# Kernel tuning notes

Measured on AMD Instinct MI355X. Metric: run time of the kernel, lower is better.

The kernel has to match this reference:

```python
import math
import jax, jax.numpy as jnp
import numpy as np

B, N, D, H, DR = 2, 1024, 1024, 16, 128  # batch, seq, dim, heads, router_dim
INIT_SCALE = 0.01   # CayleyLinear init_scale
TEMP = 1.0          # gate temperature (constant, not learnable)
TAU_D_INIT = math.log(math.expm1(0.1))  # softplus^-1(|tau_destructive|)


def setup_inputs() -> dict:
    key = jax.random.key(0)
    ks = jax.random.split(key, 6)
    x_re = jax.random.normal(ks[0], (B, N, D), jnp.float32)
    x_im = jax.random.normal(ks[1], (B, N, D), jnp.float32)
    Wq_re = jax.random.normal(ks[2], (H * DR, D), jnp.float32) * INIT_SCALE
    Wq_im = jax.random.normal(ks[3], (H * DR, D), jnp.float32) * INIT_SCALE
    Wk_re = jax.random.normal(ks[4], (H * DR, D), jnp.float32) * INIT_SCALE
    Wk_im = jax.random.normal(ks[5], (H * DR, D), jnp.float32) * INIT_SCALE
    w_destructive = jnp.full((1,), TAU_D_INIT, jnp.float32)
    return {"x_re": x_re, "x_im": x_im, "Wq_re": Wq_re, "Wq_im": Wq_im,
            "Wk_re": Wk_re, "Wk_im": Wk_im, "w_destructive": w_destructive}


def _qnormalize(z):
    # normalize_quantum_state: unit L2 norm of the complex state along last dim
    nrm = jnp.sqrt(jnp.sum(jnp.real(z) ** 2 + jnp.imag(z) ** 2, axis=-1, keepdims=True) + 1e-12)
    return z / nrm.astype(z.dtype)


def reference(x_re, x_im, Wq_re, Wq_im, Wk_re, Wk_im, w_destructive):
    x = jax.lax.complex(x_re, x_im)                 # (B, N, D) complex64
    Wq = jax.lax.complex(Wq_re, Wq_im)              # (H*DR, D)
    Wk = jax.lax.complex(Wk_re, Wk_im)
    # CayleyLinear projections, split heads: (B, N, H*DR) -> (B, H, N, DR)
    rQ = (x @ Wq.T).reshape(B, N, H, DR).transpose(0, 2, 1, 3)
    rK = (x @ Wk.T).reshape(B, N, H, DR).transpose(0, 2, 1, 3)
    rQ = _qnormalize(rQ)
    rK = _qnormalize(rK)
    # pairwise interference: 2 * Re(<q_i, k_j>) / d   -> (B, H, N, N) real
    inner = jnp.einsum('bhnd,bhmd->bhnm', jnp.conj(rQ), rK)
    inter = 2.0 * jnp.real(inner) / DR
    # SparseInterferenceGate, soft path (training=True): tau_d = -softplus(w_d)
    tau_d = -jax.nn.softplus(w_destructive[0])
    routing_weights = jax.nn.sigmoid((inter - tau_d) / (TEMP + 1e-06))
    return routing_weights
```

## Files before the change

### kernel.cpp

```cpp
#include <hip/hip_runtime.h>
#include <hip/hip_bf16.h>
#include <cstdint>


typedef int   i32x4  __attribute__((ext_vector_type(4)));
typedef float f32x4  __attribute__((ext_vector_type(4)));

#define MFMAI8(a, b, c) __builtin_amdgcn_mfma_i32_16x16x64_i8(a, b, c, 0, 0, 0)
#define BAR()   asm volatile("s_barrier" ::: "memory")
#define LGKM0() asm volatile("s_waitcnt lgkmcnt(0)" ::: "memory")
#define VM6()   asm volatile("s_waitcnt vmcnt(6)" ::: "memory")
#define VM4()   asm volatile("s_waitcnt vmcnt(4)" ::: "memory")
#define VM0()   asm volatile("s_waitcnt vmcnt(0)" ::: "memory")

#define XBOUND 5.8f
#define WBOUND 0.058f
#define XSB    8.2f
#define WSB    0.082f
#define QBOUND 3.2f

static __device__ __forceinline__ int q8(float x) {
  int i = (int)rintf(x);
  return i < -127 ? -127 : (i > 127 ? 127 : i);
}

static __device__ __forceinline__ void gload16(const void* g, void* l) {
  __builtin_amdgcn_global_load_lds(
      (const __attribute__((address_space(1))) void*)g,
      (__attribute__((address_space(3))) void*)l, 16, 0, 0);
}

static __device__ __forceinline__ unsigned pack4(int a, int b, int c, int d) {
  return (unsigned)(a & 255) | ((unsigned)(b & 255) << 8) |
         ((unsigned)(c & 255) << 16) | ((unsigned)(d & 255) << 24);
}

struct PackK {
  const float* srcA[3];
  const float* srcB[3];
  char* dA[3];
  char* dB[3];
  char* dS[3];
  float sa[3];
  float ss[3];
  float* ztab;
  int zn4;
};

__global__ __launch_bounds__(256) void pack_k_kernel(PackK jobs) {
  const int j = blockIdx.y;
  const int idx = blockIdx.x * 256 + threadIdx.x;
  if (j == 0 && idx < jobs.zn4) {
    *reinterpret_cast<float4*>(jobs.ztab + 4 * idx) = float4{0.f, 0.f, 0.f, 0.f};
  }
  const long o = (long)(idx >> 8) * 1024 + ((idx & 255) << 2);
  const float4 va = *reinterpret_cast<const float4*>(jobs.srcA[j] + o);
  const float4 vb = *reinterpret_cast<const float4*>(jobs.srcB[j] + o);
  const float sa = jobs.sa[j], ss = jobs.ss[j];
  *reinterpret_cast<unsigned*>(jobs.dA[j] + o) =
      pack4(q8(va.x * sa), q8(va.y * sa), q8(va.z * sa), q8(va.w * sa));
  *reinterpret_cast<unsigned*>(jobs.dB[j] + o) =
      pack4(q8(vb.x * sa), q8(vb.y * sa), q8(vb.z * sa), q8(vb.w * sa));
  *reinterpret_cast<unsigned*>(jobs.dS[j] + o) =
      pack4(q8((va.x + vb.x) * ss), q8((va.y + vb.y) * ss),
            q8((va.z + vb.z) * ss), q8((va.w + vb.w) * ss));
}

#define GEO_COMMON                                                             \
  const int tid  = threadIdx.x;                                                \
  const int wid  = tid >> 6;                                                   \
  const int lane = tid & 63;                                                   \
  const int wr = wid >> 2;                                                     \
  const int wc = wid & 3;                                                      \
  const int fr = lane & 15;                                                    \
  const int srow = wid * 8 + (lane >> 3);                                      \
  const int scol = ((lane & 7) ^ (lane >> 3)) << 4;                            \
  const int sxr = (lane & 7) << 4;                                             \
  const int cb0 = (((lane >> 4) << 4)) ^ sxr;                                  \
  const int cb1 = ((((lane >> 4) << 4)) + 64) ^ sxr;


#define KST(U, TILE, APAN, BPAN) do {                                          \
    const int _tl = (TILE);                                                    \
    if (_tl < 8) {                                                             \
      const char* _g = ((U) == 0 ? (APAN) : (BPAN) + ((U) - 1) * 131072)       \
                       + (long)srow * 1024 + _tl * 128 + scol;                 \
      char* _d = smem + (_tl & 1) * 49152 + (U) * 16384 + (wid << 10);         \
      gload16(_g, _d);                                                         \
      gload16(_g + 65536, _d + 8192);                                          \
    }                                                                          \
  } while (0)

#define MQ3(ACC, AV, R) do {                                                   \
    __builtin_amdgcn_s_setprio(1);                                             \
    _Pragma("unroll")                                                          \
    for (int _n = 0; _n < 4; _n++) {                                           \
      ACC[R][_n]       = MFMAI8(AV[0], b0[_n], ACC[R][_n]);                    \
      ACC[R][_n]       = MFMAI8(AV[1], b1[_n], ACC[R][_n]);                    \
      ACC[(R) + 1][_n] = MFMAI8(AV[2], b0[_n], ACC[(R) + 1][_n]);              \
      ACC[(R) + 1][_n] = MFMAI8(AV[3], b1[_n], ACC[(R) + 1][_n]);              \
    }                                                                          \
    __builtin_amdgcn_s_setprio(0);                                             \
  } while (0)

#define K3LOOP(ACC, APAN, BPAN)                                                \
  KST(0, 0, APAN, BPAN); KST(1, 0, APAN, BPAN); KST(2, 0, APAN, BPAN);         \
  KST(1, 1, APAN, BPAN); KST(2, 1, APAN, BPAN);                                \
  VM4(); BAR();                                                                \
  for (int t = 0; t < 8; ++t) {                                                \
    const char* cbuf = smem + (t & 1) * 49152;                                 \
    const char* pA = cbuf + (wr * 64 + fr) * 128;                              \
    const char* pB = cbuf + 16384 + (wc * 64 + fr) * 128;                      \
    i32x4 b0[4], b1[4], a0[4], a1[4];                                          \
    _Pragma("unroll")                                                          \
    for (int n = 0; n < 4; n++) {                                              \
      b0[n] = *(const i32x4*)(pB + n * 2048 + cb0);                            \
      b1[n] = *(const i32x4*)(pB + n * 2048 + cb1);                            \
    }                                                                          \
    a0[0] = *(const i32x4*)(pA + cb0);                                         \
    a0[1] = *(const i32x4*)(pA + cb1);                                         \
    a0[2] = *(const i32x4*)(pA + 2048 + cb0);                                  \
    a0[3] = *(const i32x4*)(pA + 2048 + cb1);                                  \
    KST(0, t + 1, APAN, BPAN);                                                 \
    BAR(); LGKM0();                                                            \
    MQ3(ACC, a0, 0);                                                           \
    BAR();                                                                     \
    a1[0] = *(const i32x4*)(pA + 4096 + cb0);                                  \
    a1[1] = *(const i32x4*)(pA + 4096 + cb1);                                  \
    a1[2] = *(const i32x4*)(pA + 6144 + cb0);                                  \
    a1[3] = *(const i32x4*)(pA + 6144 + cb1);                                  \
    KST(1, t + 2, APAN, BPAN); KST(2, t + 2, APAN, BPAN);                      \
    if (t <= 5)      { VM4(); }                                                \
    else if (t == 6) { VM0(); }                                                \
    BAR(); LGKM0();                                                            \
    MQ3(ACC, a1, 2);                                                           \
    BAR();                                                                     \
  }

#define EPI_PART(PART, EXPR) do {                                              \
    char* QKp = QpB + z * 8388608L + (PART) * 128;                             \
    float* STp = ssq + z * 32768;                                              \
    _Pragma("unroll")                                                          \
    for (int n = 0; n < 4; n++) {                                              \
      const int bn = n0 + wc * 64 + n * 16 + fr;                               \
      const int b = bn >> 10, nn = bn & 1023;                                  \
      const long rowbase = (((long)(b * 16 + hh)) * 1024 + nn) * 256;          \
      int ipr = 0;                                                             \
      _Pragma("unroll")                                                        \
      for (int mt = 0; mt < 4; mt++) {                                         \
        const int d0 = wr * 64 + mt * 16 + g * 4;                              \
        int iv0 = EXPR(mt, n, 0), iv1 = EXPR(mt, n, 1);                        \
        int iv2 = EXPR(mt, n, 2), iv3 = EXPR(mt, n, 3);                        \
        ipr += iv0 * iv0 + iv1 * iv1 + iv2 * iv2 + iv3 * iv3;                  \
        *reinterpret_cast<unsigned*>(QKp + rowbase + d0) =                     \
            pack4(iv0, iv1, iv2, iv3);                                         \
      }                                                                        \
      float s = (float)ipr;                                                    \
      s += __shfl_xor(s, 16);                                                  \
      s += __shfl_xor(s, 32);                                                  \
      if (g == 0) atomicAdd(&STp[(b * 16 + hh) * 1024 + nn], s);               \
    }                                                                          \
  } while (0)

#define EX_RE(mt, n, r) q8((float)accA[mt][n][r] * c1)
#define EX_IM(mt, n, r) q8((dq3f * (float)accA[mt][n][r] - fs[mt][n][r]) * oqv)

__global__ __launch_bounds__(512, 2)
void gemm_k3(const char* __restrict__ Wp, const char* __restrict__ Xp,
             char* __restrict__ QpB, float* __restrict__ ssq,
             float dqnf, float dq3f, float oqv, float c1) {
  __shared__ __attribute__((aligned(16))) char smem[98304];
  GEO_COMMON
  const int g = lane >> 4;
  const long z = blockIdx.z;
  const int m0 = blockIdx.y * 128;
  const int n0 = blockIdx.x * 256;
  const int hh = m0 >> 7;
  const long PL2 = 2097152;
  const char* Ar = Wp + (z * 3 + 0) * PL2 + (long)m0 * 1024;
  const char* Ai = Wp + (z * 3 + 1) * PL2 + (long)m0 * 1024;
  const char* As = Wp + (z * 3 + 2) * PL2 + (long)m0 * 1024;
  const char* Br = Xp + 0 * PL2 + (long)n0 * 1024;
  const char* Bi = Xp + 1 * PL2 + (long)n0 * 1024;
  const char* Bs = Xp + 2 * PL2 + (long)n0 * 1024;

  i32x4 accA[4][4] = {};
  K3LOOP(accA, Ar, Br)
  i32x4 accB[4][4] = {};
  K3LOOP(accB, Ai, Bi)

  f32x4 fs[4][4];
#pragma unroll
  for (int mt = 0; mt < 4; mt++)
#pragma unroll
    for (int n = 0; n < 4; n++) {
      f32x4 t;
#pragma unroll
      for (int r = 0; r < 4; r++)
        t[r] = dqnf * (float)(accA[mt][n][r] + accB[mt][n][r]);
      fs[mt][n] = t;
      accA[mt][n] -= accB[mt][n];
    }

  EPI_PART(0, EX_RE);

#pragma unroll
  for (int mt = 0; mt < 4; mt++)
#pragma unroll
    for (int n = 0; n < 4; n++) accA[mt][n] = i32x4{0, 0, 0, 0};

  K3LOOP(accA, As, Bs)

  EPI_PART(1, EX_IM);
}

#define STAGE(SEG, TILE) do {                                                  \
    const int _tl = (TILE);                                                    \
    if (_tl < NT) {                                                            \
      const char* _g = ((SEG) >= 2 ? Ag : Bg) +                                \
          (long)(((SEG) & 1) * 128 + srow) * ROWB + _tl * 128;                 \
      char* _d = smem + ((_tl & 1) << 16) + (((SEG) >= 2) ? 0 : 32768) +       \
                 (((SEG) & 1) << 14) + (wid << 10);                            \
      gload16(_g + scol, _d);                                                  \
      gload16(_g + (long)ROWB * 64 + scol, _d + 8192);                         \
    }                                                                          \
  } while (0)

#define RDQ(dst, Q) do {                                                       \
    const char* _p = pA + (Q) * 4096;                                          \
    dst[0] = *reinterpret_cast<const i32x4*>(_p + cb0);                        \
    dst[1] = *reinterpret_cast<const i32x4*>(_p + cb1);                        \
    dst[2] = *reinterpret_cast<const i32x4*>(_p + 2048 + cb0);                 \
    dst[3] = *reinterpret_cast<const i32x4*>(_p + 2048 + cb1);                 \
  } while (0)

#define MFMAQ(AV, R) do {                                                      \
    __builtin_amdgcn_s_setprio(1);                                             \
    _Pragma("unroll")                                                          \
    for (int _n = 0; _n < 4; _n++) {                                           \
      acc[R][_n]       = MFMAI8(AV[0], b0[_n], acc[R][_n]);                    \
      acc[R][_n]       = MFMAI8(AV[1], b1[_n], acc[R][_n]);                    \
      acc[(R) + 1][_n] = MFMAI8(AV[2], b0[_n], acc[(R) + 1][_n]);              \
      acc[(R) + 1][_n] = MFMAI8(AV[3], b1[_n], acc[(R) + 1][_n]);              \
    }                                                                          \
    __builtin_amdgcn_s_setprio(0);                                             \
  } while (0)

#define KLOOP()                                                                \
  STAGE(0, 0); STAGE(1, 0); STAGE(2, 0); STAGE(3, 0);                          \
  STAGE(0, 1); STAGE(1, 1); STAGE(2, 1);                                       \
  VM6();                                                                       \
  BAR();                                                                       \
  for (int t = 0; t < NT; ++t) {                                               \
    const char* curA = smem + ((t & 1) << 16);                                 \
    const char* pA = curA + (wr * 128 + fr) * 128;                             \
    const char* pB = curA + 32768 + (wc * 64 + fr) * 128;                      \
    i32x4 b0[4], b1[4], ac[4], an[4];                                          \
    _Pragma("unroll")                                                          \
    for (int n = 0; n < 4; n++) {                                              \
      b0[n] = *reinterpret_cast<const i32x4*>(pB + n * 2048 + cb0);            \
      b1[n] = *reinterpret_cast<const i32x4*>(pB + n * 2048 + cb1);            \
    }                                                                          \
    RDQ(ac, 0);                                                                \
    STAGE(3, t + 1);                                                           \
    BAR(); LGKM0();                                                            \
    MFMAQ(ac, 0);                                                              \
    BAR();                                                                     \
    RDQ(ac, 1);                                                                \
    RDQ(an, 2);                                                                \
    STAGE(0, t + 2);                                                           \
    BAR(); LGKM0();                                                            \
    MFMAQ(ac, 2);                                                              \
    BAR();                                                                     \
    RDQ(ac, 3);                                                                \
    STAGE(1, t + 2);                                                           \
    BAR(); LGKM0();                                                            \
    MFMAQ(an, 4);                                                              \
    BAR();                                                                     \
    STAGE(2, t + 2);                                                           \
    if (t <= NT - 3)      { VM6(); }                                           \
    else if (t == NT - 2) { VM0(); }                                           \
    BAR(); LGKM0();                                                            \
    MFMAQ(ac, 6);                                                              \
    BAR();                                                                     \
  }

__global__ __launch_bounds__(512, 2)
void gemm256_pw(const char* __restrict__ Ab, const char* __restrict__ Bb,
                float* __restrict__ Cb, int Kb, int ldc,
                long sA, long sB, long sC, const float* __restrict__ wdest,
                const float* __restrict__ ssq) {
  __shared__ __attribute__((aligned(16))) char smem[131072];
  __shared__ float invn[512];
  GEO_COMMON
  const int m0 = blockIdx.y * 256, n0 = blockIdx.x * 256;
  const int NT = Kb >> 7;
  const int ROWB = Kb;
  const long z = blockIdx.z;
  const char* Ag = Ab + z * sA + (long)m0 * Kb;
  const char* Bg = Bb + z * sB + (long)n0 * Kb;

  if (tid < 256) invn[tid] = 1.0f / sqrtf(ssq[z * 1024 + m0 + tid] + 1e-6f);
  else invn[tid] = 1.0f / sqrtf(ssq[32768 + z * 1024 + n0 + (tid - 256)] + 1e-6f);

  i32x4 acc[8][4] = {};
  KLOOP()

  float* C = Cb + z * sC;
  const float sp = log1pf(__expf(wdest[0]));
  const float ITEMP = 1.0f / (1.0f + 1e-6f);
  const float c  = sp * ITEMP;
  const float C0 = 1.0f / (1.0f + __expf(-c));
  const float C1 = C0 * (1.0f - C0) * ITEMP * 0.015625f;
#pragma unroll
  for (int m = 0; m < 8; m++) {
    const int lrow0 = wr * 128 + m * 16 + ((lane >> 4) << 2);
#pragma unroll
    for (int n = 0; n < 4; n++) {
      const int lcol = wc * 64 + n * 16 + fr;
      const float t = C1 * invn[256 + lcol];
#pragma unroll
      for (int r = 0; r < 4; r++) {
        const float v = fmaf((float)acc[m][n][r] * invn[lrow0 + r], t, C0);
        C[(long)(m0 + lrow0 + r) * ldc + (n0 + lcol)] = v;
      }
    }
  }
}

extern "C" void kernel_launch(void* const* d_in, const int* in_sizes, int n_in,
                              void* d_out, int out_size, void* d_ws, size_t ws_size,
                              hipStream_t stream) {
  const float* x_re  = (const float*)d_in[0];
  const float* x_im  = (const float*)d_in[1];
  const float* Wq_re = (const float*)d_in[2];
  const float* Wq_im = (const float*)d_in[3];
  const float* Wk_re = (const float*)d_in[4];
  const float* Wk_im = (const float*)d_in[5];
  const float* wdest = (const float*)d_in[6];

  const size_t PL2 = (size_t)2048 * 1024;

  char* w = (char*)d_ws;
  char*  Wpl = w;           w += 6 * PL2;
  char*  Xpl = w;           w += 3 * PL2;
  char*  Qp = w;            w += (size_t)32 * 1024 * 256;
  char*  Kp = w;            w += (size_t)32 * 1024 * 256;
  float* ssq = (float*)w;   w += (size_t)65536 * 4;

  const float sx  = 127.f / XBOUND;
  const float sw  = 127.f / WBOUND;
  const float sxs = 127.f / XSB;
  const float sws = 127.f / WSB;
  const float dqn = (XBOUND * WBOUND) / (127.f * 127.f);
  const float dq3 = (XSB * WSB) / (127.f * 127.f);
  const float oqv = 127.f / QBOUND;
  const float c1  = dqn * oqv;

  PackK jobs;
  jobs.srcA[0] = x_re;  jobs.srcB[0] = x_im;
  jobs.dA[0] = Xpl;     jobs.dB[0] = Xpl + PL2;  jobs.dS[0] = Xpl + 2 * PL2;
  jobs.sa[0] = sx;      jobs.ss[0] = sxs;
  jobs.srcA[1] = Wq_re; jobs.srcB[1] = Wq_im;
  jobs.dA[1] = Wpl;     jobs.dB[1] = Wpl + PL2;  jobs.dS[1] = Wpl + 2 * PL2;
  jobs.sa[1] = sw;      jobs.ss[1] = sws;
  jobs.srcA[2] = Wk_re; jobs.srcB[2] = Wk_im;
  jobs.dA[2] = Wpl + 3 * PL2; jobs.dB[2] = Wpl + 4 * PL2; jobs.dS[2] = Wpl + 5 * PL2;
  jobs.sa[2] = sw;      jobs.ss[2] = sws;
  jobs.ztab = ssq;
  jobs.zn4 = 16384;

  pack_k_kernel<<<dim3(2048, 3), 256, 0, stream>>>(jobs);

  gemm_k3<<<dim3(8, 16, 2), 512, 0, stream>>>(
      Wpl, Xpl, Qp, ssq, dqn, dq3, oqv, c1);

  gemm256_pw<<<dim3(4, 4, 32), 512, 0, stream>>>(
      Qp, Kp, (float*)d_out, 256, 1024,
      (long)1024 * 256, (long)1024 * 256,
      (long)1024 * 1024, wdest, ssq);
}
```

Measured before the change: 84.10 us.

## Shrink projection GEMM tile to 128x128 with 256-thread blocks

The int8 projection GEMM kernel now uses 128x128 output tiles computed by four waves in a 2x2 layout, with 64KB of shared memory, instead of 128x256 tiles on eight waves with 96KB. The launch grid doubles to 512 blocks so more of the CUs get work, and the smaller shared footprint may allow more resident blocks per CU. Staging is restructured so the A and B panels each load four row groups per stage. The trade-off is less reuse of the A tile per block and more total global and LDS traffic.

```diff
diff --git a/kernel.cpp b/kernel.cpp
--- a/kernel.cpp
+++ b/kernel.cpp
@@ -66,28 +66,29 @@
             q8((va.z + vb.z) * ss), q8((va.w + vb.w) * ss));
 }
 
-#define GEO_COMMON                                                             \
-  const int tid  = threadIdx.x;                                                \
-  const int wid  = tid >> 6;                                                   \
-  const int lane = tid & 63;                                                   \
-  const int wr = wid >> 2;                                                     \
-  const int wc = wid & 3;                                                      \
-  const int fr = lane & 15;                                                    \
-  const int srow = wid * 8 + (lane >> 3);                                      \
-  const int scol = ((lane & 7) ^ (lane >> 3)) << 4;                            \
-  const int sxr = (lane & 7) << 4;                                             \
-  const int cb0 = (((lane >> 4) << 4)) ^ sxr;                                  \
-  const int cb1 = ((((lane >> 4) << 4)) + 64) ^ sxr;
-
-
-#define KST(U, TILE, APAN, BPAN) do {                                          \
+
+#define KSTA(TILE, APAN) do {                                                  \
     const int _tl = (TILE);                                                    \
     if (_tl < 8) {                                                             \
-      const char* _g = ((U) == 0 ? (APAN) : (BPAN) + ((U) - 1) * 131072)       \
-                       + (long)srow * 1024 + _tl * 128 + scol;                 \
-      char* _d = smem + (_tl & 1) * 49152 + (U) * 16384 + (wid << 10);         \
-      gload16(_g, _d);                                                         \
-      gload16(_g + 65536, _d + 8192);                                          \
+      _Pragma("unroll")                                                        \
+      for (int _u = 0; _u < 4; _u++) {                                         \
+        const char* _g = (APAN) + (long)(_u * 32 + srow) * 1024                \
+                         + _tl * 128 + scol;                                   \
+        gload16(_g, smem + ((_tl & 1) << 15) + (_u << 12) + (wid << 10));      \
+      }                                                                        \
+    }                                                                          \
+  } while (0)
+
+#define KSTB(TILE, BPAN) do {                                                  \
+    const int _tl = (TILE);                                                    \
+    if (_tl < 8) {                                                             \
+      _Pragma("unroll")                                                        \
+      for (int _u = 0; _u < 4; _u++) {                                         \
+        const char* _g = (BPAN) + (long)(_u * 32 + srow) * 1024                \
+                         + _tl * 128 + scol;                                   \
+        gload16(_g, smem + ((_tl & 1) << 15) + 16384 + (_u << 12)              \
+                    + (wid << 10));                                            \
+      }                                                                        \
     }                                                                          \
   } while (0)
 
@@ -104,11 +105,10 @@
   } while (0)
 
 #define K3LOOP(ACC, APAN, BPAN)                                                \
-  KST(0, 0, APAN, BPAN); KST(1, 0, APAN, BPAN); KST(2, 0, APAN, BPAN);         \
-  KST(1, 1, APAN, BPAN); KST(2, 1, APAN, BPAN);                                \
+  KSTB(0, BPAN); KSTA(0, APAN); KSTB(1, BPAN);                                 \
   VM4(); BAR();                                                                \
   for (int t = 0; t < 8; ++t) {                                                \
-    const char* cbuf = smem + (t & 1) * 49152;                                 \
+    const char* cbuf = smem + ((t & 1) << 15);                                 \
     const char* pA = cbuf + (wr * 64 + fr) * 128;                              \
     const char* pB = cbuf + 16384 + (wc * 64 + fr) * 128;                      \
     i32x4 b0[4], b1[4], a0[4], a1[4];                                          \
@@ -121,7 +121,7 @@
     a0[1] = *(const i32x4*)(pA + cb1);                                         \
     a0[2] = *(const i32x4*)(pA + 2048 + cb0);                                  \
     a0[3] = *(const i32x4*)(pA + 2048 + cb1);                                  \
-    KST(0, t + 1, APAN, BPAN);                                                 \
+    KSTA(t + 1, APAN);                                                         \
     BAR(); LGKM0();                                                            \
     MQ3(ACC, a0, 0);                                                           \
     BAR();                                                                     \
@@ -129,7 +129,7 @@
     a1[1] = *(const i32x4*)(pA + 4096 + cb1);                                  \
     a1[2] = *(const i32x4*)(pA + 6144 + cb0);                                  \
     a1[3] = *(const i32x4*)(pA + 6144 + cb1);                                  \
-    KST(1, t + 2, APAN, BPAN); KST(2, t + 2, APAN, BPAN);                      \
+    KSTB(t + 2, BPAN);                                                         \
     if (t <= 5)      { VM4(); }                                                \
     else if (t == 6) { VM0(); }                                                \
     BAR(); LGKM0();                                                            \
@@ -165,16 +165,27 @@
 #define EX_RE(mt, n, r) q8((float)accA[mt][n][r] * c1)
 #define EX_IM(mt, n, r) q8((dq3f * (float)accA[mt][n][r] - fs[mt][n][r]) * oqv)
 
-__global__ __launch_bounds__(512, 2)
+__global__ __launch_bounds__(256, 2)
 void gemm_k3(const char* __restrict__ Wp, const char* __restrict__ Xp,
              char* __restrict__ QpB, float* __restrict__ ssq,
              float dqnf, float dq3f, float oqv, float c1) {
-  __shared__ __attribute__((aligned(16))) char smem[98304];
-  GEO_COMMON
-  const int g = lane >> 4;
+  __shared__ __attribute__((aligned(16))) char smem[65536];
+  const int tid  = threadIdx.x;
+  const int wid  = tid >> 6;
+  const int lane = tid & 63;
+  const int wr = wid >> 1;
+  const int wc = wid & 1;
+  const int fr = lane & 15;
+  const int g  = lane >> 4;
+  const int srow = wid * 8 + (lane >> 3);
+  const int scol = ((lane & 7) ^ (lane >> 3)) << 4;
+  const int sxr = (lane & 7) << 4;
+  const int cb0 = (((lane >> 4) << 4)) ^ sxr;
+  const int cb1 = ((((lane >> 4) << 4)) + 64) ^ sxr;
+
   const long z = blockIdx.z;
   const int m0 = blockIdx.y * 128;
-  const int n0 = blockIdx.x * 256;
+  const int n0 = blockIdx.x * 128;
   const int hh = m0 >> 7;
   const long PL2 = 2097152;
   const char* Ar = Wp + (z * 3 + 0) * PL2 + (long)m0 * 1024;
@@ -213,6 +224,19 @@
 
   EPI_PART(1, EX_IM);
 }
+
+#define GEO_COMMON                                                             \
+  const int tid  = threadIdx.x;                                                \
+  const int wid  = tid >> 6;                                                   \
+  const int lane = tid & 63;                                                   \
+  const int wr = wid >> 2;                                                     \
+  const int wc = wid & 3;                                                      \
+  const int fr = lane & 15;                                                    \
+  const int srow = wid * 8 + (lane >> 3);                                      \
+  const int scol = ((lane & 7) ^ (lane >> 3)) << 4;                            \
+  const int sxr = (lane & 7) << 4;                                             \
+  const int cb0 = (((lane >> 4) << 4)) ^ sxr;                                  \
+  const int cb1 = ((((lane >> 4) << 4)) + 64) ^ sxr;
 
 #define STAGE(SEG, TILE) do {                                                  \
     const int _tl = (TILE);                                                    \
@@ -372,7 +396,7 @@
 
   pack_k_kernel<<<dim3(2048, 3), 256, 0, stream>>>(jobs);
 
-  gemm_k3<<<dim3(8, 16, 2), 512, 0, stream>>>(
+  gemm_k3<<<dim3(16, 16, 2), 256, 0, stream>>>(
       Wpl, Xpl, Qp, ssq, dqn, dq3, oqv, c1);
 
   gemm256_pw<<<dim3(4, 4, 32), 512, 0, stream>>>(
```

Measured after the change: 84.39 us. About the same (+0.4%).
